# Performance work log

Measured on AMD Instinct MI355X. Metric: run time of the kernel, lower is better.

Reference implementation:

```python
import jax, jax.numpy as jnp
import numpy as np

B, S, D, H = 2, 2048, 1024, 16
HD = D // H
DFF = 4 * D
EPS = 1e-5


def layernorm(x, g, b):
    mu = jnp.mean(x, axis=-1, keepdims=True)
    var = jnp.mean((x - mu) ** 2, axis=-1, keepdims=True)
    return (x - mu) * jax.lax.rsqrt(var + EPS) * g + b


def setup_inputs() -> dict:
    key = jax.random.key(0)
    ks = jax.random.split(key, 16)
    sc = 0.02
    return {
        "x": jax.random.normal(ks[0], (B, S, D), jnp.float32),
        "pos_emb": jax.random.normal(ks[1], (S, D), jnp.float32),
        "ln1_g": jnp.ones((D,), jnp.float32),
        "ln1_b": jnp.zeros((D,), jnp.float32),
        "w_qkv": jax.random.normal(ks[2], (D, 3 * D), jnp.float32) * sc,
        "b_qkv": jnp.zeros((3 * D,), jnp.float32),
        "w_o": jax.random.normal(ks[3], (D, D), jnp.float32) * sc,
        "b_o": jnp.zeros((D,), jnp.float32),
        "ln2_g": jnp.ones((D,), jnp.float32),
        "ln2_b": jnp.zeros((D,), jnp.float32),
        "w_fc": jax.random.normal(ks[4], (D, DFF), jnp.float32) * sc,
        "b_fc": jnp.zeros((DFF,), jnp.float32),
        "w_proj": jax.random.normal(ks[5], (DFF, D), jnp.float32) * sc,
        "b_proj": jnp.zeros((D,), jnp.float32),
    }


def reference(x, pos_emb, ln1_g, ln1_b, w_qkv, b_qkv, w_o, b_o,
              ln2_g, ln2_b, w_fc, b_fc, w_proj, b_proj):
    # --- attention sub-block: x + attn(norm1(x) + pos_emb) ---
    h = layernorm(x, ln1_g, ln1_b) + pos_emb  # [B,S,D]
    qkv = h @ w_qkv + b_qkv                    # [B,S,3D]
    qkv = qkv.reshape(B, S, 3, H, HD).transpose(2, 0, 3, 1, 4)  # [3,B,H,S,HD]
    q, k, v = qkv[0], qkv[1], qkv[2]
    # naive full attention: materialize [B,H,S,S]
    w = jnp.einsum('bhqd,bhkd->bhqk', q, k) / jnp.sqrt(jnp.float32(HD))
    causal = jnp.tril(jnp.ones((S, S), bool))  # True = keep
    w = jnp.where(causal, w, -jnp.inf)
    a = jax.nn.softmax(w, axis=-1)
    out = jnp.einsum('bhqk,bhkd->bhqd', a, v)   # [B,H,S,HD]
    out = out.transpose(0, 2, 1, 3).reshape(B, S, D)
    x = x + out @ w_o + b_o
    # --- MLP sub-block: x + mlp(norm2(x)) ---
    m = layernorm(x, ln2_g, ln2_b)
    m = jax.nn.gelu(m @ w_fc + b_fc) @ w_proj + b_proj
    return x + m
```

## Files before the change

### kernel.cpp

```cpp
#include <hip/hip_runtime.h>
#include <hip/hip_bf16.h>

typedef __hip_bfloat16 bf16_t;
typedef __bf16 bf16x8 __attribute__((ext_vector_type(8)));
typedef float f32x4 __attribute__((ext_vector_type(4)));

__device__ __forceinline__ void gload_lds16(const void* g, void* l) {
  __builtin_amdgcn_global_load_lds(
      (const __attribute__((address_space(1))) void*)g,
      (__attribute__((address_space(3))) void*)l, 16, 0, 0);
}

__device__ __forceinline__ unsigned short f2bf(float f) {
  bf16_t h = __float2bfloat16(f);
  return reinterpret_cast<unsigned short&>(h);
}

__global__ __launch_bounds__(256) void wtrans_kernel(
    const float* __restrict__ in, bf16_t* __restrict__ out, int K, int N) {
  __shared__ float tile[32][33];
  int tx = threadIdx.x, ty = threadIdx.y;
  int n = blockIdx.x * 32 + tx;
  int k0 = blockIdx.y * 32 + ty;
#pragma unroll
  for (int j = 0; j < 32; j += 8) tile[ty + j][tx] = in[(size_t)(k0 + j) * N + n];
  __syncthreads();
  int k = blockIdx.y * 32 + tx;
  int n0 = blockIdx.x * 32 + ty;
#pragma unroll
  for (int j = 0; j < 32; j += 8)
    out[(size_t)(n0 + j) * K + k] = __float2bfloat16(tile[tx][ty + j]);
}

__global__ __launch_bounds__(256) void ln_kernel(
    const float* __restrict__ x, const float* __restrict__ g,
    const float* __restrict__ b, const float* __restrict__ pos,
    bf16_t* __restrict__ out, int S) {
  int row = blockIdx.x;
  int tid = threadIdx.x;
  const float4* xr = (const float4*)(x + (size_t)row * 1024);
  float4 v = xr[tid];
  float s1 = v.x + v.y + v.z + v.w;
  float s2 = v.x * v.x + v.y * v.y + v.z * v.z + v.w * v.w;
#pragma unroll
  for (int off = 1; off < 64; off <<= 1) {
    s1 += __shfl_xor(s1, off);
    s2 += __shfl_xor(s2, off);
  }
  __shared__ float red[2][4];
  int w = tid >> 6;
  if ((tid & 63) == 0) { red[0][w] = s1; red[1][w] = s2; }
  __syncthreads();
  s1 = red[0][0] + red[0][1] + red[0][2] + red[0][3];
  s2 = red[1][0] + red[1][1] + red[1][2] + red[1][3];
  float mu = s1 * (1.f / 1024.f);
  float var = s2 * (1.f / 1024.f) - mu * mu;
  float rs = rsqrtf(var + 1e-5f);
  float4 gg = ((const float4*)g)[tid];
  float4 bb = ((const float4*)b)[tid];
  float4 pp = {0.f, 0.f, 0.f, 0.f};
  if (pos) pp = ((const float4*)(pos + (size_t)(row & (S - 1)) * 1024))[tid];
  ushort4 o4;
  o4.x = f2bf((v.x - mu) * rs * gg.x + bb.x + pp.x);
  o4.y = f2bf((v.y - mu) * rs * gg.y + bb.y + pp.y);
  o4.z = f2bf((v.z - mu) * rs * gg.z + bb.z + pp.z);
  o4.w = f2bf((v.w - mu) * rs * gg.w + bb.w + pp.w);
  ((ushort4*)(out + (size_t)row * 1024))[tid] = o4;
}

template <int EPI, int DBUF>
__global__ __launch_bounds__(256) void gemm_bt(
    const bf16_t* __restrict__ A, const bf16_t* __restrict__ BT,
    const float* __restrict__ bias, const float* __restrict__ resid,
    float* __restrict__ outf, bf16_t* __restrict__ outb,
    bf16_t* __restrict__ qb, bf16_t* __restrict__ kb, bf16_t* __restrict__ vb,
    int M, int N, int K) {
  __shared__ char lds[DBUF ? 65536 : 32768];
  int tid = threadIdx.x;
  int l = tid & 63;
  int w = tid >> 6;
  int wr = w >> 1, wc = w & 1;
  int ll = l & 15, lg = l >> 4;
  int rowBase = blockIdx.y * 128, colBase = blockIdx.x * 128;

  f32x4 acc[4][4];
  f32x4 z = {0.f, 0.f, 0.f, 0.f};
#pragma unroll
  for (int i = 0; i < 4; i++)
#pragma unroll
    for (int j = 0; j < 4; j++) acc[i][j] = z;

  auto STAGE = [&](int kt, int c) {
#pragma unroll
    for (int i = 0; i < 4; i++) {
      int p = i * 4096 + tid * 16;
      int o = p ^ (((p >> 7) & 7) << 4);
      int r = o >> 7, cc = (o & 127) >> 1;
      gload_lds16(A + (size_t)(rowBase + r) * K + kt * 64 + cc, lds + c * 32768 + p);
    }
#pragma unroll
    for (int i = 0; i < 4; i++) {
      int p = i * 4096 + tid * 16;
      int o = p ^ (((p >> 7) & 7) << 4);
      int r = o >> 7, cc = (o & 127) >> 1;
      gload_lds16(BT + (size_t)(colBase + r) * K + kt * 64 + cc,
                  lds + c * 32768 + 16384 + p);
    }
  };

  int nkt = K >> 6;
  if (DBUF) STAGE(0, 0);
  int cbuf = 0;
  for (int kt = 0; kt < nkt; ++kt) {
    if (DBUF) {
      __builtin_amdgcn_s_barrier();
      if (kt + 1 < nkt) {
        STAGE(kt + 1, cbuf ^ 1);
        asm volatile("s_waitcnt vmcnt(8)" ::: "memory");
      } else {
        asm volatile("s_waitcnt vmcnt(0)" ::: "memory");
      }
      __builtin_amdgcn_s_barrier();
      asm volatile("" ::: "memory");
    } else {
      __syncthreads();
      STAGE(kt, 0);
      __syncthreads();
    }
    char* Ab = lds + cbuf * 32768;
    char* Bb = Ab + 16384;

    bf16x8 af[4][2], bfv[4][2];
#pragma unroll
    for (int mi = 0; mi < 4; mi++) {
      int row = wr * 64 + mi * 16 + ll;
#pragma unroll
      for (int kk = 0; kk < 2; kk++) {
        int o = (row << 7) + (kk << 6) + (lg << 4);
        af[mi][kk] = *(const bf16x8*)(Ab + (o ^ ((row & 7) << 4)));
      }
    }
#pragma unroll
    for (int ni = 0; ni < 4; ni++) {
      int row = wc * 64 + ni * 16 + ll;
#pragma unroll
      for (int kk = 0; kk < 2; kk++) {
        int o = (row << 7) + (kk << 6) + (lg << 4);
        bfv[ni][kk] = *(const bf16x8*)(Bb + (o ^ ((row & 7) << 4)));
      }
    }
#pragma unroll
    for (int mi = 0; mi < 4; mi++)
#pragma unroll
      for (int ni = 0; ni < 4; ni++)
#pragma unroll
        for (int kk = 0; kk < 2; kk++)
          acc[mi][ni] = __builtin_amdgcn_mfma_f32_16x16x32_bf16(
              af[mi][kk], bfv[ni][kk], acc[mi][ni], 0, 0, 0);
    if (DBUF) cbuf ^= 1;
  }

#pragma unroll
  for (int mi = 0; mi < 4; mi++) {
#pragma unroll
    for (int ni = 0; ni < 4; ni++) {
#pragma unroll
      for (int j = 0; j < 4; j++) {
        int grow = rowBase + wr * 64 + mi * 16 + lg * 4 + j;
        int gcol = colBase + wc * 64 + ni * 16 + ll;
        float v = acc[mi][ni][j] + bias[gcol];
        if (EPI == 0) {
          int bb = grow >> 11, s = grow & 2047;
          int t = gcol >> 10, rem = gcol & 1023;
          int h = rem >> 6, d = rem & 63;
          size_t bh = (size_t)(bb * 16 + h);
          if (t == 0)
            qb[(bh * 2048 + s) * 64 + d] = __float2bfloat16(v);
          else if (t == 1)
            kb[(bh * 2048 + s) * 64 + d] = __float2bfloat16(v);
          else
            vb[(bh * 64 + d) * 2048 + s] = __float2bfloat16(v);
        } else if (EPI == 1) {
          size_t idx = (size_t)grow * N + gcol;
          outf[idx] = resid[idx] + v;
        } else {
          float c3 = v * v * v;
          float t = tanhf(0.7978845608028654f * (v + 0.044715f * c3));
          outb[(size_t)grow * N + gcol] = __float2bfloat16(0.5f * v * (1.f + t));
        }
      }
    }
  }
}

__global__ __launch_bounds__(256, 2) void attn_kernel(
    const bf16_t* __restrict__ qb, const bf16_t* __restrict__ kb,
    const bf16_t* __restrict__ vbT, bf16_t* __restrict__ op, int S) {
  int id = blockIdx.x;
  int bh = id & 31;
  int qt = 15 - (id >> 5);
  int tid = threadIdx.x;
  int w = tid >> 6, l = tid & 63;
  int ll = l & 15, lg = l >> 4;
  __shared__ char lds[49152];
  char* Pw = lds + 32768 + w * 4096;

  int qbase = qt * 128;
  int qlo = qbase + w * 32;
  int qhi = qlo + 31;

  bf16x8 qf[2][2];
#pragma unroll
  for (int mi = 0; mi < 2; mi++) {
    const bf16_t* qrp = qb + ((size_t)bh * S + qbase + w * 32 + mi * 16 + ll) * 64;
#pragma unroll
    for (int kk = 0; kk < 2; kk++) qf[mi][kk] = *(const bf16x8*)(qrp + kk * 32 + lg * 8);
  }

  f32x4 Oacc[2][4];
  f32x4 z = {0.f, 0.f, 0.f, 0.f};
#pragma unroll
  for (int mi = 0; mi < 2; mi++)
#pragma unroll
    for (int i = 0; i < 4; i++) Oacc[mi][i] = z;
  float mrow[2][4], lrow[2][4];
#pragma unroll
  for (int mi = 0; mi < 2; mi++)
#pragma unroll
    for (int j = 0; j < 4; j++) { mrow[mi][j] = -INFINITY; lrow[mi][j] = 0.f; }

  int last = 2 * qt + 1;

  auto STAGE = [&](int kt, int c) {
    char* Kt = lds + c * 8192;
    char* Vt = lds + 16384 + c * 8192;
#pragma unroll
    for (int i = 0; i < 2; ++i) {
      int p = i * 4096 + tid * 16;
      int o = p ^ (((p >> 7) & 7) << 4);
      int r = o >> 7, cc = (o & 127) >> 1;
      gload_lds16(kb + ((size_t)bh * S + kt * 64 + r) * 64 + cc, Kt + p);
    }
#pragma unroll
    for (int i = 0; i < 2; ++i) {
      int p = i * 4096 + tid * 16;
      int o = p ^ (((p >> 7) & 7) << 4);
      int d = o >> 7, cc = (o & 127) >> 1;
      gload_lds16(vbT + ((size_t)bh * 64 + d) * S + kt * 64 + cc, Vt + p);
    }
  };

  STAGE(0, 0);
  int c = 0;
  for (int kt = 0; kt <= last; ++kt) {
    __builtin_amdgcn_s_barrier();
    if (kt < last) {
      STAGE(kt + 1, c ^ 1);
      asm volatile("s_waitcnt vmcnt(4)" ::: "memory");
    } else {
      asm volatile("s_waitcnt vmcnt(0)" ::: "memory");
    }
    __builtin_amdgcn_s_barrier();
    asm volatile("" ::: "memory");

    if (kt * 64 <= qhi) {
      char* Kt = lds + c * 8192;
      char* Vt = lds + 16384 + c * 8192;

      bf16x8 kf[4][2];
#pragma unroll
      for (int f = 0; f < 4; f++) {
        int row = f * 16 + ll;
#pragma unroll
        for (int kk = 0; kk < 2; kk++) {
          int o = (row << 7) + (kk << 6) + (lg << 4);
          kf[f][kk] = *(const bf16x8*)(Kt + (o ^ ((row & 7) << 4)));
        }
      }
      f32x4 sfr[2][4];
#pragma unroll
      for (int mi = 0; mi < 2; mi++)
#pragma unroll
        for (int f = 0; f < 4; f++) {
          sfr[mi][f] = z;
#pragma unroll
          for (int kk = 0; kk < 2; kk++)
            sfr[mi][f] = __builtin_amdgcn_mfma_f32_16x16x32_bf16(
                qf[mi][kk], kf[f][kk], sfr[mi][f], 0, 0, 0);
        }

      bool diag = (kt * 64 + 63) > qlo;
#pragma unroll
      for (int mi = 0; mi < 2; mi++) {
#pragma unroll
        for (int j = 0; j < 4; j++) {
          int qr = qlo + mi * 16 + lg * 4 + j;
          float mx = -INFINITY;
#pragma unroll
          for (int f = 0; f < 4; f++) {
            float s = sfr[mi][f][j] * 0.125f;
            if (diag && (kt * 64 + f * 16 + ll) > qr) s = -INFINITY;
            sfr[mi][f][j] = s;
            mx = fmaxf(mx, s);
          }
#pragma unroll
          for (int off = 1; off < 16; off <<= 1) mx = fmaxf(mx, __shfl_xor(mx, off));
          float mnew = fmaxf(mrow[mi][j], mx);
          float fj = __expf(mrow[mi][j] - mnew);
          float sum = 0.f;
#pragma unroll
          for (int f = 0; f < 4; f++) {
            float p = __expf(sfr[mi][f][j] - mnew);
            sfr[mi][f][j] = p;
            sum += p;
          }
#pragma unroll
          for (int off = 1; off < 16; off <<= 1) sum += __shfl_xor(sum, off);
          lrow[mi][j] = lrow[mi][j] * fj + sum;
          mrow[mi][j] = mnew;
#pragma unroll
          for (int fd = 0; fd < 4; fd++) Oacc[mi][fd][j] *= fj;
        }
      }

#pragma unroll
      for (int mi = 0; mi < 2; mi++)
#pragma unroll
        for (int j = 0; j < 4; j++) {
          int r = mi * 16 + lg * 4 + j;
#pragma unroll
          for (int f = 0; f < 4; f++) {
            int o = (r << 7) + ((f * 16 + ll) << 1);
            *(unsigned short*)(Pw + (o ^ ((r & 7) << 4))) = f2bf(sfr[mi][f][j]);
          }
        }

      bf16x8 vf2[4][2];
#pragma unroll
      for (int fd = 0; fd < 4; fd++) {
        int row = fd * 16 + ll;
#pragma unroll
        for (int kk = 0; kk < 2; kk++) {
          int o = (row << 7) + (kk << 6) + (lg << 4);
          vf2[fd][kk] = *(const bf16x8*)(Vt + (o ^ ((row & 7) << 4)));
        }
      }
      bf16x8 pf[2][2];
#pragma unroll
      for (int mi = 0; mi < 2; mi++) {
        int pr = mi * 16 + ll;
#pragma unroll
        for (int kk = 0; kk < 2; kk++) {
          int o = (pr << 7) + (kk << 6) + (lg << 4);
          pf[mi][kk] = *(const bf16x8*)(Pw + (o ^ ((pr & 7) << 4)));
        }
      }
#pragma unroll
      for (int mi = 0; mi < 2; mi++)
#pragma unroll
        for (int fd = 0; fd < 4; fd++)
#pragma unroll
          for (int kk = 0; kk < 2; kk++)
            Oacc[mi][fd] = __builtin_amdgcn_mfma_f32_16x16x32_bf16(
                pf[mi][kk], vf2[fd][kk], Oacc[mi][fd], 0, 0, 0);
    }
    c ^= 1;
  }

  int b = bh >> 4, hh = bh & 15;
#pragma unroll
  for (int mi = 0; mi < 2; mi++)
#pragma unroll
    for (int j = 0; j < 4; j++) {
      int srow = qbase + w * 32 + mi * 16 + lg * 4 + j;
      float inv = 1.f / lrow[mi][j];
#pragma unroll
      for (int fd = 0; fd < 4; fd++) {
        int col = (hh << 6) + (fd << 4) + ll;
        op[((size_t)b * S + srow) * 1024 + col] = __float2bfloat16(Oacc[mi][fd][j] * inv);
      }
    }
}

extern "C" void kernel_launch(void* const* d_in, const int* in_sizes, int n_in,
                              void* d_out, int out_size, void* d_ws, size_t ws_size,
                              hipStream_t stream) {
  const float* x = (const float*)d_in[0];
  const float* pos_emb = (const float*)d_in[1];
  const float* ln1_g = (const float*)d_in[2];
  const float* ln1_b = (const float*)d_in[3];
  const float* w_qkv = (const float*)d_in[4];
  const float* b_qkv = (const float*)d_in[5];
  const float* w_o = (const float*)d_in[6];
  const float* b_o = (const float*)d_in[7];
  const float* ln2_g = (const float*)d_in[8];
  const float* ln2_b = (const float*)d_in[9];
  const float* w_fc = (const float*)d_in[10];
  const float* b_fc = (const float*)d_in[11];
  const float* w_proj = (const float*)d_in[12];
  const float* b_proj = (const float*)d_in[13];

  char* ws = (char*)d_ws;
  auto take = [&](size_t bytes) {
    char* p = ws;
    ws += (bytes + 255) & ~(size_t)255;
    return p;
  };
  bf16_t* wqkvT = (bf16_t*)take(3072ull * 1024 * 2);
  bf16_t* woT = (bf16_t*)take(1024ull * 1024 * 2);
  bf16_t* wfcT = (bf16_t*)take(4096ull * 1024 * 2);
  bf16_t* wprojT = (bf16_t*)take(1024ull * 4096 * 2);
  bf16_t* h = (bf16_t*)take(4096ull * 1024 * 2);
  bf16_t* qbuf = (bf16_t*)take(32ull * 2048 * 64 * 2);
  bf16_t* kbuf = (bf16_t*)take(32ull * 2048 * 64 * 2);
  bf16_t* vbuf = (bf16_t*)take(32ull * 2048 * 64 * 2);
  bf16_t* aout = (bf16_t*)take(4096ull * 1024 * 2);
  float* x2 = (float*)take(4096ull * 1024 * 4);
  bf16_t* mb = (bf16_t*)take(4096ull * 1024 * 2);
  bf16_t* fca = (bf16_t*)qbuf;

  dim3 tb(32, 8);
  wtrans_kernel<<<dim3(3072 / 32, 1024 / 32), tb, 0, stream>>>(w_qkv, wqkvT, 1024, 3072);
  wtrans_kernel<<<dim3(1024 / 32, 1024 / 32), tb, 0, stream>>>(w_o, woT, 1024, 1024);
  wtrans_kernel<<<dim3(4096 / 32, 1024 / 32), tb, 0, stream>>>(w_fc, wfcT, 1024, 4096);
  wtrans_kernel<<<dim3(1024 / 32, 4096 / 32), tb, 0, stream>>>(w_proj, wprojT, 4096, 1024);

  ln_kernel<<<4096, 256, 0, stream>>>(x, ln1_g, ln1_b, pos_emb, h, 2048);

  gemm_bt<0, 0><<<dim3(24, 32), 256, 0, stream>>>(h, wqkvT, b_qkv, nullptr, nullptr,
                                                  nullptr, qbuf, kbuf, vbuf, 4096, 3072, 1024);

  attn_kernel<<<dim3(512), 256, 0, stream>>>(qbuf, kbuf, vbuf, aout, 2048);

  gemm_bt<1, 1><<<dim3(8, 32), 256, 0, stream>>>(aout, woT, b_o, x, x2, nullptr,
                                                 nullptr, nullptr, nullptr, 4096, 1024, 1024);

  ln_kernel<<<4096, 256, 0, stream>>>(x2, ln2_g, ln2_b, nullptr, mb, 2048);

  gemm_bt<2, 0><<<dim3(32, 32), 256, 0, stream>>>(mb, wfcT, b_fc, nullptr, nullptr,
                                                  fca, nullptr, nullptr, nullptr, 4096, 4096, 1024);

  gemm_bt<1, 1><<<dim3(8, 32), 256, 0, stream>>>(fca, wprojT, b_proj, x2, (float*)d_out,
                                                 nullptr, nullptr, nullptr, nullptr, 4096, 1024, 4096);
}
```

Before: 417.2 us.

## Swizzle GEMM block order for XCDs and restructure attention softmax with lazy rescale

The GEMMs now launch on a 1D grid and remap block IDs so that consecutive tiles land on the same XCD chiplet, aiming for better L2 reuse. The attention kernel swaps the MFMA operands so each lane holds a whole query row. That cuts the row max and sum reductions from four shuffle steps to two and lets P be written to LDS as packed 8-byte stores. It also skips rescaling the running max and accumulators unless the new max grows by more than 8, and raises wave priority around the MFMA sections. The lazy rescale lets exponentials reach up to e^8 before renormalising, which slightly changes the numerics.

```diff
diff --git a/kernel.cpp b/kernel.cpp
--- a/kernel.cpp
+++ b/kernel.cpp
@@ -81,7 +81,11 @@
   int w = tid >> 6;
   int wr = w >> 1, wc = w & 1;
   int ll = l & 15, lg = l >> 4;
-  int rowBase = blockIdx.y * 128, colBase = blockIdx.x * 128;
+  int chunk = gridDim.x >> 3;
+  int swz = (blockIdx.x & 7) * chunk + (blockIdx.x >> 3);
+  int nbx = N >> 7;
+  int bx = swz % nbx, by = swz / nbx;
+  int rowBase = by * 128, colBase = bx * 128;
 
   f32x4 acc[4][4];
   f32x4 z = {0.f, 0.f, 0.f, 0.f};
@@ -223,11 +227,9 @@
   for (int mi = 0; mi < 2; mi++)
 #pragma unroll
     for (int i = 0; i < 4; i++) Oacc[mi][i] = z;
-  float mrow[2][4], lrow[2][4];
-#pragma unroll
-  for (int mi = 0; mi < 2; mi++)
-#pragma unroll
-    for (int j = 0; j < 4; j++) { mrow[mi][j] = -INFINITY; lrow[mi][j] = 0.f; }
+  float mrow[2], lrow[2];
+#pragma unroll
+  for (int mi = 0; mi < 2; mi++) { mrow[mi] = -INFINITY; lrow[mi] = 0.f; }
 
   int last = 2 * qt + 1;
 
@@ -278,6 +280,7 @@
         }
       }
       f32x4 sfr[2][4];
+      __builtin_amdgcn_s_setprio(1);
 #pragma unroll
       for (int mi = 0; mi < 2; mi++)
 #pragma unroll
@@ -286,54 +289,68 @@
 #pragma unroll
           for (int kk = 0; kk < 2; kk++)
             sfr[mi][f] = __builtin_amdgcn_mfma_f32_16x16x32_bf16(
-                qf[mi][kk], kf[f][kk], sfr[mi][f], 0, 0, 0);
-        }
+                kf[f][kk], qf[mi][kk], sfr[mi][f], 0, 0, 0);
+        }
+      __builtin_amdgcn_s_setprio(0);
 
       bool diag = (kt * 64 + 63) > qlo;
+      float mx[2];
 #pragma unroll
       for (int mi = 0; mi < 2; mi++) {
-#pragma unroll
-        for (int j = 0; j < 4; j++) {
-          int qr = qlo + mi * 16 + lg * 4 + j;
-          float mx = -INFINITY;
-#pragma unroll
-          for (int f = 0; f < 4; f++) {
+        int gq = qlo + mi * 16 + ll;
+        float m_ = -INFINITY;
+#pragma unroll
+        for (int f = 0; f < 4; f++)
+#pragma unroll
+          for (int j = 0; j < 4; j++) {
             float s = sfr[mi][f][j] * 0.125f;
-            if (diag && (kt * 64 + f * 16 + ll) > qr) s = -INFINITY;
+            if (diag && (kt * 64 + f * 16 + lg * 4 + j) > gq) s = -INFINITY;
             sfr[mi][f][j] = s;
-            mx = fmaxf(mx, s);
+            m_ = fmaxf(m_, s);
           }
-#pragma unroll
-          for (int off = 1; off < 16; off <<= 1) mx = fmaxf(mx, __shfl_xor(mx, off));
-          float mnew = fmaxf(mrow[mi][j], mx);
-          float fj = __expf(mrow[mi][j] - mnew);
-          float sum = 0.f;
-#pragma unroll
-          for (int f = 0; f < 4; f++) {
-            float p = __expf(sfr[mi][f][j] - mnew);
-            sfr[mi][f][j] = p;
-            sum += p;
+        m_ = fmaxf(m_, __shfl_xor(m_, 16));
+        m_ = fmaxf(m_, __shfl_xor(m_, 32));
+        mx[mi] = m_;
+      }
+
+      bool ok = (mx[0] <= mrow[0] + 8.f) && (mx[1] <= mrow[1] + 8.f);
+      if (!__all(ok)) {
+#pragma unroll
+        for (int mi = 0; mi < 2; mi++) {
+          float mnew = fmaxf(mrow[mi], mx[mi]);
+          float fj = __expf(mrow[mi] - mnew);
+          mrow[mi] = mnew;
+          lrow[mi] *= fj;
+#pragma unroll
+          for (int j = 0; j < 4; j++) {
+            float frow = __shfl(fj, (lg << 2) + j);
+#pragma unroll
+            for (int fd = 0; fd < 4; fd++) Oacc[mi][fd][j] *= frow;
           }
-#pragma unroll
-          for (int off = 1; off < 16; off <<= 1) sum += __shfl_xor(sum, off);
-          lrow[mi][j] = lrow[mi][j] * fj + sum;
-          mrow[mi][j] = mnew;
-#pragma unroll
-          for (int fd = 0; fd < 4; fd++) Oacc[mi][fd][j] *= fj;
-        }
-      }
-
-#pragma unroll
-      for (int mi = 0; mi < 2; mi++)
-#pragma unroll
-        for (int j = 0; j < 4; j++) {
-          int r = mi * 16 + lg * 4 + j;
-#pragma unroll
-          for (int f = 0; f < 4; f++) {
-            int o = (r << 7) + ((f * 16 + ll) << 1);
-            *(unsigned short*)(Pw + (o ^ ((r & 7) << 4))) = f2bf(sfr[mi][f][j]);
-          }
-        }
+        }
+      }
+
+#pragma unroll
+      for (int mi = 0; mi < 2; mi++) {
+        float sum = 0.f;
+        int q = mi * 16 + ll;
+#pragma unroll
+        for (int f = 0; f < 4; f++) {
+          float p0 = __expf(sfr[mi][f][0] - mrow[mi]);
+          float p1 = __expf(sfr[mi][f][1] - mrow[mi]);
+          float p2 = __expf(sfr[mi][f][2] - mrow[mi]);
+          float p3 = __expf(sfr[mi][f][3] - mrow[mi]);
+          sum += (p0 + p1) + (p2 + p3);
+          uint2 pk;
+          pk.x = (unsigned)f2bf(p0) | ((unsigned)f2bf(p1) << 16);
+          pk.y = (unsigned)f2bf(p2) | ((unsigned)f2bf(p3) << 16);
+          int o = (q << 7) + ((f * 16 + lg * 4) << 1);
+          *(uint2*)(Pw + (o ^ ((q & 7) << 4))) = pk;
+        }
+        sum += __shfl_xor(sum, 16);
+        sum += __shfl_xor(sum, 32);
+        lrow[mi] += sum;
+      }
 
       bf16x8 vf2[4][2];
 #pragma unroll
@@ -355,6 +372,7 @@
           pf[mi][kk] = *(const bf16x8*)(Pw + (o ^ ((pr & 7) << 4)));
         }
       }
+      __builtin_amdgcn_s_setprio(1);
 #pragma unroll
       for (int mi = 0; mi < 2; mi++)
 #pragma unroll
@@ -363,23 +381,26 @@
           for (int kk = 0; kk < 2; kk++)
             Oacc[mi][fd] = __builtin_amdgcn_mfma_f32_16x16x32_bf16(
                 pf[mi][kk], vf2[fd][kk], Oacc[mi][fd], 0, 0, 0);
+      __builtin_amdgcn_s_setprio(0);
     }
     c ^= 1;
   }
 
   int b = bh >> 4, hh = bh & 15;
 #pragma unroll
-  for (int mi = 0; mi < 2; mi++)
+  for (int mi = 0; mi < 2; mi++) {
+    float invA = 1.f / lrow[mi];
 #pragma unroll
     for (int j = 0; j < 4; j++) {
+      float inv = __shfl(invA, (lg << 2) + j);
       int srow = qbase + w * 32 + mi * 16 + lg * 4 + j;
-      float inv = 1.f / lrow[mi][j];
 #pragma unroll
       for (int fd = 0; fd < 4; fd++) {
         int col = (hh << 6) + (fd << 4) + ll;
         op[((size_t)b * S + srow) * 1024 + col] = __float2bfloat16(Oacc[mi][fd][j] * inv);
       }
     }
+  }
 }
 
 extern "C" void kernel_launch(void* const* d_in, const int* in_sizes, int n_in,
@@ -427,19 +448,19 @@
 
   ln_kernel<<<4096, 256, 0, stream>>>(x, ln1_g, ln1_b, pos_emb, h, 2048);
 
-  gemm_bt<0, 0><<<dim3(24, 32), 256, 0, stream>>>(h, wqkvT, b_qkv, nullptr, nullptr,
-                                                  nullptr, qbuf, kbuf, vbuf, 4096, 3072, 1024);
+  gemm_bt<0, 0><<<dim3(768), 256, 0, stream>>>(h, wqkvT, b_qkv, nullptr, nullptr,
+                                               nullptr, qbuf, kbuf, vbuf, 4096, 3072, 1024);
 
   attn_kernel<<<dim3(512), 256, 0, stream>>>(qbuf, kbuf, vbuf, aout, 2048);
 
-  gemm_bt<1, 1><<<dim3(8, 32), 256, 0, stream>>>(aout, woT, b_o, x, x2, nullptr,
-                                                 nullptr, nullptr, nullptr, 4096, 1024, 1024);
+  gemm_bt<1, 1><<<dim3(256), 256, 0, stream>>>(aout, woT, b_o, x, x2, nullptr,
+                                               nullptr, nullptr, nullptr, 4096, 1024, 1024);
 
   ln_kernel<<<4096, 256, 0, stream>>>(x2, ln2_g, ln2_b, nullptr, mb, 2048);
 
-  gemm_bt<2, 0><<<dim3(32, 32), 256, 0, stream>>>(mb, wfcT, b_fc, nullptr, nullptr,
-                                                  fca, nullptr, nullptr, nullptr, 4096, 4096, 1024);
-
-  gemm_bt<1, 1><<<dim3(8, 32), 256, 0, stream>>>(fca, wprojT, b_proj, x2, (float*)d_out,
-                                                 nullptr, nullptr, nullptr, nullptr, 4096, 1024, 4096);
-}
+  gemm_bt<2, 0><<<dim3(1024), 256, 0, stream>>>(mb, wfcT, b_fc, nullptr, nullptr,
+                                                fca, nullptr, nullptr, nullptr, 4096, 4096, 1024);
+
+  gemm_bt<1, 1><<<dim3(256), 256, 0, stream>>>(fca, wprojT, b_proj, x2, (float*)d_out,
+                                               nullptr, nullptr, nullptr, nullptr, 4096, 1024, 4096);
+}
```

Result: faster. 380.5 us (-8.8%).
